# Optimization experiments

Hardware: AMD Instinct MI355X
Metric: run time of the kernel (lower is better)

## Reference

```python
import jax, jax.numpy as jnp
import numpy as np

E, KD, VD = 1024, 1024, 1024
B, S = 4, 4096


def setup_inputs() -> dict:
    key = jax.random.key(0)
    ks = jax.random.split(key, 7)
    sE, sK = 1.0 / np.sqrt(E), 1.0 / np.sqrt(E)
    return {
        "x": jax.random.normal(ks[0], (B, S, E), dtype=jnp.float32),
        "Wq": jax.random.normal(ks[1], (E, KD), dtype=jnp.float32) * sE,
        "bq": jnp.zeros((KD,), dtype=jnp.float32),
        "Wk": jax.random.normal(ks[2], (E, KD), dtype=jnp.float32) * sE,
        "bk": jnp.zeros((KD,), dtype=jnp.float32),
        "Wv": jax.random.normal(ks[3], (E, VD), dtype=jnp.float32) * sE,
        "bv": jnp.zeros((VD,), dtype=jnp.float32),
    }


def reference(x, Wq, bq, Wk, bk, Wv, bv):
    # Separate Q/K/V projections (nn.Linear equivalents)
    Q = jnp.einsum("bse,ek->bsk", x, Wq) + bq  # [B,S,KD]
    K = jnp.einsum("bse,ek->bsk", x, Wk) + bk  # [B,S,KD]
    V = jnp.einsum("bse,ev->bsv", x, Wv) + bv  # [B,S,VD]
    scale = 1.0 / jnp.sqrt(jnp.float32(KD))
    scores = jnp.einsum("bqk,bsk->bqs", Q, K) * scale  # [B,S,S]
    attn = jax.nn.softmax(scores, axis=-1)
    out = jnp.einsum("bqs,bsv->bqv", attn, V)  # [B,S,VD]
    return out
```

## Files before the change

kernel.cpp:

```cpp
#include <hip/hip_runtime.h>
#include <cstdint>
#include <math.h>

typedef __attribute__((ext_vector_type(8))) short short8;
typedef __attribute__((ext_vector_type(4))) float f32x4;

#define AS1C const __attribute__((address_space(1))) void*
#define AS3  __attribute__((address_space(3))) void*

__device__ __forceinline__ unsigned short f2bf(float f) {
  union { float f; unsigned int u; } v; v.f = f;
  unsigned int r = v.u + 0x7FFFu + ((v.u >> 16) & 1u);
  return (unsigned short)(r >> 16);
}

__global__ void cast_x_kernel(const float* __restrict__ x, unsigned short* __restrict__ xb) {
  int i = blockIdx.x * blockDim.x + threadIdx.x;
  float4 v = ((const float4*)x)[i];
  ushort4 o;
  o.x = f2bf(v.x); o.y = f2bf(v.y); o.z = f2bf(v.z); o.w = f2bf(v.w);
  ((ushort4*)xb)[i] = o;
}

__global__ void zero_f4_kernel(float4* __restrict__ o) {
  size_t i = (size_t)blockIdx.x * blockDim.x + threadIdx.x;
  float4 z; z.x = 0.f; z.y = 0.f; z.z = 0.f; z.w = 0.f;
  o[i] = z;
}

__global__ void transpose_cast_kernel(const float* __restrict__ W0, const float* __restrict__ W1,
                                      const float* __restrict__ W2,
                                      unsigned short* __restrict__ T0, unsigned short* __restrict__ T1,
                                      unsigned short* __restrict__ T2) {
  __shared__ float tile[32][33];
  const float* W = (blockIdx.z == 0) ? W0 : (blockIdx.z == 1 ? W1 : W2);
  unsigned short* T = (blockIdx.z == 0) ? T0 : (blockIdx.z == 1 ? T1 : T2);
  int tx = threadIdx.x & 31, ty = threadIdx.x >> 5;
  int bx = blockIdx.x * 32, by = blockIdx.y * 32;
#pragma unroll
  for (int i = 0; i < 32; i += 8)
    tile[ty + i][tx] = W[(size_t)(by + ty + i) * 1024 + bx + tx];
  __syncthreads();
#pragma unroll
  for (int i = 0; i < 32; i += 8)
    T[(size_t)(bx + ty + i) * 1024 + by + tx] = f2bf(tile[tx][ty + i]);
}

template <int KDIM, int NT>
__device__ __forceinline__ void gemm_core(const unsigned short* __restrict__ Abase,
                                          const unsigned short* __restrict__ Btbase,
                                          unsigned short* smem, f32x4 acc[8][4]) {
  constexpr int BK = 32;
  const int t = threadIdx.x;
  const int lane = t & 63, wave = t >> 6;
  const int wm = wave >> 2, wn = wave & 3;
  const int quad = lane >> 4, l16 = lane & 15;

  const int row0 = t >> 3;
  const int gsw = (t & 7) ^ (row0 & 7);
  const unsigned short* gsrc =
      (gsw & 4) ? (Btbase + (size_t)row0 * KDIM + (size_t)(gsw - 4) * 8)
                : (Abase + (size_t)row0 * KDIM + (size_t)gsw * 8);

  auto stage = [&](int tt) {
    unsigned short* buf = smem + (tt & 3) * 16384;
    const unsigned short* s = gsrc + tt * BK;
#pragma unroll
    for (int j = 0; j < 4; ++j)
      __builtin_amdgcn_global_load_lds((AS1C)(s + (size_t)j * 64 * KDIM),
                                       (AS3)(buf + (t + j * 512) * 8), 16, 0, 0);
  };

  stage(0);
  stage(1);
  stage(2);

  for (int tt = 0; tt < NT; ++tt) {
    if (tt < NT - 2)       asm volatile("s_waitcnt vmcnt(8)\n\ts_barrier" ::: "memory");
    else if (tt == NT - 2) asm volatile("s_waitcnt vmcnt(4)\n\ts_barrier" ::: "memory");
    else                   asm volatile("s_waitcnt vmcnt(0)\n\ts_barrier" ::: "memory");
    if (tt + 3 < NT) stage(tt + 3);

    const unsigned short* buf = smem + (tt & 3) * 16384;
    short8 a[8], b[4];
#pragma unroll
    for (int ni = 0; ni < 4; ++ni) {
      int row = wn * 64 + ni * 16 + l16;
      b[ni] = *(const short8*)(buf + row * 64 + (((4 + quad) ^ (row & 7)) << 3));
    }
#pragma unroll
    for (int mi = 0; mi < 8; ++mi) {
      int row = wm * 128 + mi * 16 + l16;
      a[mi] = *(const short8*)(buf + row * 64 + ((quad ^ (row & 7)) << 3));
    }
    __builtin_amdgcn_s_setprio(1);
#pragma unroll
    for (int mi = 0; mi < 8; ++mi)
#pragma unroll
      for (int ni = 0; ni < 4; ++ni)
        acc[mi][ni] = __builtin_amdgcn_mfma_f32_16x16x32_bf16(a[mi], b[ni], acc[mi][ni], 0, 0, 0);
    __builtin_amdgcn_s_setprio(0);
  }
}

struct ProjArgs {
  const unsigned short* bt[3];
  const float* bias[3];
  unsigned short* c[3];
};
struct SPairArgs {
  const unsigned short* q[2];
  const unsigned short* k[2];
  unsigned short* pc[2][4];
  float* rs[2];
};
struct PVPairArgs {
  const unsigned short* pc[2][4];
  const unsigned short* vt[2];
  const float* rs[2];
  float* out[2];
};

__global__ __launch_bounds__(512, 2) void gemm256_proj(
    const unsigned short* __restrict__ A, ProjArgs pa) {
  extern __shared__ unsigned short smem[];
  const int t = threadIdx.x;
  const int lane = t & 63, wave = t >> 6;
  const int wm = wave >> 2, wn = wave & 3;
  const int quad = lane >> 4, l16 = lane & 15;
  const int z = blockIdx.z;

  const int gx = gridDim.x;
  const int nwg = gx * gridDim.y;
  int bid = blockIdx.y * gx + blockIdx.x;
  bid = (bid & 7) * (nwg >> 3) + (bid >> 3);
  const int bx = bid % gx, by = bid / gx;
  const int m0 = bx * 256, n0 = by * 256;

  f32x4 acc[8][4];
  const f32x4 fz = {0.f, 0.f, 0.f, 0.f};
#pragma unroll
  for (int mi = 0; mi < 8; ++mi)
#pragma unroll
    for (int ni = 0; ni < 4; ++ni) acc[mi][ni] = fz;

  gemm_core<1024, 32>(A + (size_t)m0 * 1024, pa.bt[z] + (size_t)n0 * 1024, smem, acc);

  const float* bias = pa.bias[z];
  unsigned short* C = pa.c[z];
  const float scale = (z == 0) ? 0.03125f : 1.0f;
  if (z < 2) {
#pragma unroll
    for (int mi = 0; mi < 8; ++mi) {
      int row = m0 + wm * 128 + mi * 16 + quad * 4;
#pragma unroll
      for (int ni = 0; ni < 4; ++ni) {
        int col = n0 + wn * 64 + ni * 16 + l16;
        float bv = bias[col];
#pragma unroll
        for (int r = 0; r < 4; ++r)
          C[(size_t)(row + r) * 1024 + col] = f2bf((acc[mi][ni][r] + bv) * scale);
      }
    }
  } else {
#pragma unroll
    for (int mi = 0; mi < 8; ++mi) {
      int row = m0 + wm * 128 + mi * 16 + quad * 4;
      int bb = row >> 12, ss = row & 4095;
#pragma unroll
      for (int ni = 0; ni < 4; ++ni) {
        int col = n0 + wn * 64 + ni * 16 + l16;
        float bv = bias[col];
        ushort4 pk;
        pk.x = f2bf(acc[mi][ni][0] + bv);
        pk.y = f2bf(acc[mi][ni][1] + bv);
        pk.z = f2bf(acc[mi][ni][2] + bv);
        pk.w = f2bf(acc[mi][ni][3] + bv);
        *(ushort4*)&C[((size_t)bb * 1024 + col) * 4096 + ss] = pk;
      }
    }
  }
}

__global__ __launch_bounds__(512, 2) void gemm256_s(SPairArgs sa) {
  extern __shared__ unsigned short smem[];
  const int t = threadIdx.x;
  const int lane = t & 63, wave = t >> 6;
  const int wm = wave >> 2, wn = wave & 3;
  const int quad = lane >> 4, l16 = lane & 15;
  const int z = blockIdx.z;

  const int gx = gridDim.x;
  const int nwg = gx * gridDim.y;
  int bid = blockIdx.y * gx + blockIdx.x;
  bid = (bid & 7) * (nwg >> 3) + (bid >> 3);
  const int bx = bid % gx, by = bid / gx;
  const int m0 = bx * 256, n0 = by * 256;

  f32x4 acc[8][4];
  const f32x4 fz = {0.f, 0.f, 0.f, 0.f};
#pragma unroll
  for (int mi = 0; mi < 8; ++mi)
#pragma unroll
    for (int ni = 0; ni < 4; ++ni) acc[mi][ni] = fz;

  gemm_core<1024, 32>(sa.q[z] + (size_t)m0 * 1024, sa.k[z] + (size_t)n0 * 1024, smem, acc);

  unsigned short* base = sa.pc[z][m0 >> 10];
  float* rs = sa.rs[z];
#pragma unroll
  for (int mi = 0; mi < 8; ++mi) {
    int row = m0 + wm * 128 + mi * 16 + quad * 4;
    int rowl = row & 1023;
    float pr[4] = {0.f, 0.f, 0.f, 0.f};
#pragma unroll
    for (int ni = 0; ni < 4; ++ni) {
      int col = n0 + wn * 64 + ni * 16 + l16;
#pragma unroll
      for (int r = 0; r < 4; ++r) {
        float p = __expf(acc[mi][ni][r]);
        base[(size_t)(rowl + r) * 4096 + col] = f2bf(p);
        pr[r] += p;
      }
    }
#pragma unroll
    for (int r = 0; r < 4; ++r) {
      float v = pr[r];
      v += __shfl_xor(v, 1);
      v += __shfl_xor(v, 2);
      v += __shfl_xor(v, 4);
      v += __shfl_xor(v, 8);
      if (l16 == 0) atomicAdd(&rs[row + r], v);
    }
  }
}

__global__ __launch_bounds__(512, 2) void gemm256_pv(PVPairArgs va) {
  extern __shared__ unsigned short smem[];
  const int t = threadIdx.x;
  const int lane = t & 63, wave = t >> 6;
  const int wm = wave >> 2, wn = wave & 3;
  const int quad = lane >> 4, l16 = lane & 15;
  const int z = blockIdx.z;

  const int gx = gridDim.x, gy = gridDim.y;
  const int nwg = gx * gy;
  int lid = blockIdx.y * gx + blockIdx.x;
  int s = (lid & 7) * (nwg >> 3) + (lid >> 3);
  const int bx = s / gy, by = s % gy;
  const int m0 = bx * 256, n0 = by * 256;

  f32x4 acc[8][4];
  const f32x4 fz = {0.f, 0.f, 0.f, 0.f};
#pragma unroll
  for (int mi = 0; mi < 8; ++mi)
#pragma unroll
    for (int ni = 0; ni < 4; ++ni) acc[mi][ni] = fz;

  const unsigned short* Abase = va.pc[z][m0 >> 10] + (size_t)(m0 & 1023) * 4096;
  gemm_core<4096, 128>(Abase, va.vt[z] + (size_t)n0 * 4096, smem, acc);

  const float* rs = va.rs[z];
  float* outp = va.out[z];
#pragma unroll
  for (int mi = 0; mi < 8; ++mi) {
    int row = m0 + wm * 128 + mi * 16 + quad * 4;
    float inv[4];
#pragma unroll
    for (int r = 0; r < 4; ++r) inv[r] = 1.0f / rs[row + r];
#pragma unroll
    for (int ni = 0; ni < 4; ++ni) {
      int col = n0 + wn * 64 + ni * 16 + l16;
#pragma unroll
      for (int r = 0; r < 4; ++r)
        outp[(size_t)(row + r) * 1024 + col] = acc[mi][ni][r] * inv[r];
    }
  }
}

extern "C" void kernel_launch(void* const* d_in, const int* in_sizes, int n_in,
                              void* d_out, int out_size, void* d_ws, size_t ws_size,
                              hipStream_t stream) {
  const float* x  = (const float*)d_in[0];
  const float* Wq = (const float*)d_in[1];
  const float* bq = (const float*)d_in[2];
  const float* Wk = (const float*)d_in[3];
  const float* bk = (const float*)d_in[4];
  const float* Wv = (const float*)d_in[5];
  const float* bv = (const float*)d_in[6];
  float* out = (float*)d_out;

  const size_t MR = (size_t)16384 * 1024;
  const size_t SB = (size_t)4096 * 1024;
  unsigned short* xb  = (unsigned short*)d_ws;
  unsigned short* Qb  = xb + MR;
  unsigned short* Kb  = Qb + MR;
  unsigned short* Vtb = Kb + MR;
  unsigned short* WqT = Vtb + MR;
  unsigned short* WkT = WqT + (size_t)1024 * 1024;
  unsigned short* WvT = WkT + (size_t)1024 * 1024;
  float* rs = (float*)WqT;
  unsigned short* outU = (unsigned short*)(out + (size_t)2 * 4096 * 1024);

  hipFuncSetAttribute((const void*)gemm256_proj,
                      hipFuncAttributeMaxDynamicSharedMemorySize, 131072);
  hipFuncSetAttribute((const void*)gemm256_s,
                      hipFuncAttributeMaxDynamicSharedMemorySize, 131072);
  hipFuncSetAttribute((const void*)gemm256_pv,
                      hipFuncAttributeMaxDynamicSharedMemorySize, 131072);

  cast_x_kernel<<<16384, 256, 0, stream>>>(x, xb);
  transpose_cast_kernel<<<dim3(32, 32, 3), 256, 0, stream>>>(Wq, Wk, Wv, WqT, WkT, WvT);

  ProjArgs pa;
  pa.bt[0] = WqT;  pa.bt[1] = WkT;  pa.bt[2] = WvT;
  pa.bias[0] = bq; pa.bias[1] = bk; pa.bias[2] = bv;
  pa.c[0] = Qb;    pa.c[1] = Kb;    pa.c[2] = Vtb;
  gemm256_proj<<<dim3(64, 4, 3), 512, 131072, stream>>>(xb, pa);

  zero_f4_kernel<<<16, 256, 0, stream>>>((float4*)rs);

  SPairArgs sA;
  sA.q[0] = Qb;      sA.k[0] = Kb;      sA.rs[0] = rs;
  sA.q[1] = Qb + SB; sA.k[1] = Kb + SB; sA.rs[1] = rs + 4096;
  for (int c = 0; c < 4; ++c) { sA.pc[0][c] = xb + (size_t)c * SB; sA.pc[1][c] = outU + (size_t)c * SB; }
  gemm256_s<<<dim3(16, 16, 2), 512, 131072, stream>>>(sA);

  PVPairArgs vA;
  for (int c = 0; c < 4; ++c) { vA.pc[0][c] = sA.pc[0][c]; vA.pc[1][c] = sA.pc[1][c]; }
  vA.vt[0] = Vtb;      vA.rs[0] = rs;        vA.out[0] = out;
  vA.vt[1] = Vtb + SB; vA.rs[1] = rs + 4096; vA.out[1] = out + (size_t)4096 * 1024;
  gemm256_pv<<<dim3(16, 4, 2), 512, 131072, stream>>>(vA);

  SPairArgs sB;
  sB.q[0] = Qb + 2 * SB; sB.k[0] = Kb + 2 * SB; sB.rs[0] = rs + 2 * 4096;
  sB.q[1] = Qb + 3 * SB; sB.k[1] = Kb + 3 * SB; sB.rs[1] = rs + 3 * 4096;
  for (int c = 0; c < 4; ++c) sB.pc[0][c] = xb + (size_t)c * SB;
  sB.pc[1][0] = Qb; sB.pc[1][1] = Qb + SB; sB.pc[1][2] = Kb; sB.pc[1][3] = Kb + SB;
  gemm256_s<<<dim3(16, 16, 2), 512, 131072, stream>>>(sB);

  PVPairArgs vB;
  for (int c = 0; c < 4; ++c) { vB.pc[0][c] = sB.pc[0][c]; vB.pc[1][c] = sB.pc[1][c]; }
  vB.vt[0] = Vtb + 2 * SB; vB.rs[0] = rs + 2 * 4096; vB.out[0] = out + (size_t)2 * 4096 * 1024;
  vB.vt[1] = Vtb + 3 * SB; vB.rs[1] = rs + 3 * 4096; vB.out[1] = out + (size_t)3 * 4096 * 1024;
  gemm256_pv<<<dim3(16, 4, 2), 512, 131072, stream>>>(vB);
}
```

Baseline: 612.0 us.

## Restructure GEMM mainloop into 8-phase ping-pong schedule with half-K LDS regions

Replaces the 4-stage BK=32 GEMM pipeline with a schedule that processes BK=64 per iteration split into two half-K LDS regions. Each iteration is interleaved in phases that alternate LDS reads of half the A fragments, issue global→LDS loads, and run 16-MFMA bursts between barriers. The LDS layout changes to 32-element rows with a 4-way XOR swizzle. The goal is finer-grained overlap of memory traffic with MFMA work and fewer stalls per K-step, at the cost of many more barriers per iteration and tighter waitcnt bookkeeping.

```diff
diff --git a/kernel.cpp b/kernel.cpp
--- a/kernel.cpp
+++ b/kernel.cpp
@@ -47,60 +47,123 @@
 }
 
 template <int KDIM, int NT>
-__device__ __forceinline__ void gemm_core(const unsigned short* __restrict__ Abase,
-                                          const unsigned short* __restrict__ Btbase,
-                                          unsigned short* smem, f32x4 acc[8][4]) {
-  constexpr int BK = 32;
+__device__ __forceinline__ void gemm_core8(const unsigned short* __restrict__ Abase,
+                                           const unsigned short* __restrict__ Btbase,
+                                           unsigned short* smem, f32x4 acc[8][4]) {
   const int t = threadIdx.x;
   const int lane = t & 63, wave = t >> 6;
   const int wm = wave >> 2, wn = wave & 3;
   const int quad = lane >> 4, l16 = lane & 15;
 
-  const int row0 = t >> 3;
-  const int gsw = (t & 7) ^ (row0 & 7);
-  const unsigned short* gsrc =
-      (gsw & 4) ? (Btbase + (size_t)row0 * KDIM + (size_t)(gsw - 4) * 8)
-                : (Abase + (size_t)row0 * KDIM + (size_t)gsw * 8);
-
-  auto stage = [&](int tt) {
-    unsigned short* buf = smem + (tt & 3) * 16384;
-    const unsigned short* s = gsrc + tt * BK;
-#pragma unroll
-    for (int j = 0; j < 4; ++j)
-      __builtin_amdgcn_global_load_lds((AS1C)(s + (size_t)j * 64 * KDIM),
-                                       (AS3)(buf + (t + j * 512) * 8), 16, 0, 0);
+  const unsigned short* srcp[4];
+  int dstoff[4];
+#pragma unroll
+  for (int s = 0; s < 4; ++s) {
+    int gi = t + s * 512;
+    int idx = gi & 1023;
+    int row = idx >> 2;
+    int sg = (idx & 3) ^ (row & 3);
+    srcp[s] = ((gi >> 10) ? Btbase : Abase) + (size_t)row * KDIM + sg * 8;
+    dstoff[s] = gi * 8;
+  }
+
+  auto stage2 = [&](int reg, int T, int h, int pair) {
+    unsigned short* buf = smem + reg * 16384;
+#pragma unroll
+    for (int s2 = 0; s2 < 2; ++s2) {
+      int s = pair * 2 + s2;
+      __builtin_amdgcn_global_load_lds((AS1C)(srcp[s] + T * 64 + h * 32),
+                                       (AS3)(buf + dstoff[s]), 16, 0, 0);
+    }
   };
-
-  stage(0);
-  stage(1);
-  stage(2);
-
-  for (int tt = 0; tt < NT; ++tt) {
-    if (tt < NT - 2)       asm volatile("s_waitcnt vmcnt(8)\n\ts_barrier" ::: "memory");
-    else if (tt == NT - 2) asm volatile("s_waitcnt vmcnt(4)\n\ts_barrier" ::: "memory");
-    else                   asm volatile("s_waitcnt vmcnt(0)\n\ts_barrier" ::: "memory");
-    if (tt + 3 < NT) stage(tt + 3);
-
-    const unsigned short* buf = smem + (tt & 3) * 16384;
-    short8 a[8], b[4];
-#pragma unroll
-    for (int ni = 0; ni < 4; ++ni) {
-      int row = wn * 64 + ni * 16 + l16;
-      b[ni] = *(const short8*)(buf + row * 64 + (((4 + quad) ^ (row & 7)) << 3));
-    }
-#pragma unroll
-    for (int mi = 0; mi < 8; ++mi) {
-      int row = wm * 128 + mi * 16 + l16;
-      a[mi] = *(const short8*)(buf + row * 64 + ((quad ^ (row & 7)) << 3));
-    }
+  auto rdA4 = [&](short8* a, int reg, int mb) {
+    const unsigned short* buf = smem + reg * 16384;
+#pragma unroll
+    for (int i = 0; i < 4; ++i) {
+      int row = wm * 128 + (mb + i) * 16 + l16;
+      a[i] = *(const short8*)(buf + row * 32 + ((quad ^ (row & 3)) << 3));
+    }
+  };
+  auto rdB4 = [&](short8* b, int reg) {
+    const unsigned short* buf = smem + reg * 16384 + 8192;
+#pragma unroll
+    for (int i = 0; i < 4; ++i) {
+      int row = wn * 64 + i * 16 + l16;
+      b[i] = *(const short8*)(buf + row * 32 + ((quad ^ (row & 3)) << 3));
+    }
+  };
+  auto mf16 = [&](short8* a, short8* b, int mb) {
     __builtin_amdgcn_s_setprio(1);
 #pragma unroll
-    for (int mi = 0; mi < 8; ++mi)
+    for (int mi = 0; mi < 4; ++mi)
 #pragma unroll
       for (int ni = 0; ni < 4; ++ni)
-        acc[mi][ni] = __builtin_amdgcn_mfma_f32_16x16x32_bf16(a[mi], b[ni], acc[mi][ni], 0, 0, 0);
+        acc[mb + mi][ni] =
+            __builtin_amdgcn_mfma_f32_16x16x32_bf16(a[mi], b[ni], acc[mb + mi][ni], 0, 0, 0);
     __builtin_amdgcn_s_setprio(0);
+  };
+
+#define BAR()   asm volatile("s_barrier" ::: "memory")
+#define LGKM0() asm volatile("s_waitcnt lgkmcnt(0)" ::: "memory")
+#define VM(N)   asm volatile("s_waitcnt vmcnt(" #N ")" ::: "memory")
+
+  stage2(0, 0, 0, 0); stage2(0, 0, 0, 1);
+  stage2(1, 0, 1, 0); stage2(1, 0, 1, 1);
+  stage2(2, 1, 0, 0); stage2(2, 1, 0, 1);
+  VM(8);
+  BAR();
+
+  short8 a0[4], a1[4], b0[4];
+  for (int it = 0; it < NT / 2; ++it) {
+    const int T = 2 * it;
+    const bool lastI = (it == NT / 2 - 1);
+    rdA4(a0, 0, 0); rdB4(b0, 0);
+    stage2(3, T + 1, 1, 0);
+    BAR(); LGKM0();
+    mf16(a0, b0, 0);
+    BAR();
+    rdA4(a1, 0, 4);
+    stage2(3, T + 1, 1, 1);
+    VM(8);
+    BAR(); LGKM0();
+    mf16(a1, b0, 4);
+    BAR();
+    rdA4(a0, 1, 0); rdB4(b0, 1);
+    if (!lastI) stage2(0, T + 2, 0, 0);
+    BAR(); LGKM0();
+    mf16(a0, b0, 0);
+    BAR();
+    rdA4(a1, 1, 4);
+    if (!lastI) { stage2(0, T + 2, 0, 1); VM(8); }
+    else        { VM(4); }
+    BAR(); LGKM0();
+    mf16(a1, b0, 4);
+    BAR();
+    rdA4(a0, 2, 0); rdB4(b0, 2);
+    if (!lastI) stage2(1, T + 2, 1, 0);
+    BAR(); LGKM0();
+    mf16(a0, b0, 0);
+    BAR();
+    rdA4(a1, 2, 4);
+    if (!lastI) { stage2(1, T + 2, 1, 1); VM(8); }
+    else        { VM(0); }
+    BAR(); LGKM0();
+    mf16(a1, b0, 4);
+    BAR();
+    rdA4(a0, 3, 0); rdB4(b0, 3);
+    if (!lastI) stage2(2, T + 3, 0, 0);
+    BAR(); LGKM0();
+    mf16(a0, b0, 0);
+    BAR();
+    rdA4(a1, 3, 4);
+    if (!lastI) { stage2(2, T + 3, 0, 1); VM(8); }
+    BAR(); LGKM0();
+    mf16(a1, b0, 4);
+    BAR();
   }
+#undef BAR
+#undef LGKM0
+#undef VM
 }
 
 struct ProjArgs {
@@ -144,7 +207,7 @@
 #pragma unroll
     for (int ni = 0; ni < 4; ++ni) acc[mi][ni] = fz;
 
-  gemm_core<1024, 32>(A + (size_t)m0 * 1024, pa.bt[z] + (size_t)n0 * 1024, smem, acc);
+  gemm_core8<1024, 16>(A + (size_t)m0 * 1024, pa.bt[z] + (size_t)n0 * 1024, smem, acc);
 
   const float* bias = pa.bias[z];
   unsigned short* C = pa.c[z];
@@ -204,7 +267,7 @@
 #pragma unroll
     for (int ni = 0; ni < 4; ++ni) acc[mi][ni] = fz;
 
-  gemm_core<1024, 32>(sa.q[z] + (size_t)m0 * 1024, sa.k[z] + (size_t)n0 * 1024, smem, acc);
+  gemm_core8<1024, 16>(sa.q[z] + (size_t)m0 * 1024, sa.k[z] + (size_t)n0 * 1024, smem, acc);
 
   unsigned short* base = sa.pc[z][m0 >> 10];
   float* rs = sa.rs[z];
@@ -258,7 +321,7 @@
     for (int ni = 0; ni < 4; ++ni) acc[mi][ni] = fz;
 
   const unsigned short* Abase = va.pc[z][m0 >> 10] + (size_t)(m0 & 1023) * 4096;
-  gemm_core<4096, 128>(Abase, va.vt[z] + (size_t)n0 * 4096, smem, acc);
+  gemm_core8<4096, 64>(Abase, va.vt[z] + (size_t)n0 * 4096, smem, acc);
 
   const float* rs = va.rs[z];
   float* outp = va.out[z];
```

Measured after the change: 628.3 us. +2.7%, slower.
